# Optimization experiments

Measured on AMD Instinct MI355X. Metric: run time of the kernel, lower is better.

Reference implementation:

```python
import jax, jax.numpy as jnp
import numpy as np

V, T, B = 32000, 64, 32
H, E = 32, 200


def setup_inputs() -> dict:
    key = jax.random.key(0)
    ks = jax.random.split(key, 9)
    s = lambda *d: 1.0 / np.sqrt(d[-1])
    return {
        "y": jax.random.randint(ks[0], (B, T), 0, V, dtype=jnp.int64) if jax.config.jax_enable_x64 else jax.random.randint(ks[0], (B, T), 0, V, dtype=jnp.int32),
        "encoder_last_hidden": jax.random.normal(ks[1], (B, H), dtype=jnp.float32),
        "emb_table": jax.random.normal(ks[2], (V, E), dtype=jnp.float32),
        "Wi": jax.random.uniform(ks[3], (H, E), jnp.float32, -s(E), s(E)),
        "bi": jax.random.uniform(ks[4], (H,), jnp.float32, -s(E), s(E)),
        "Wh": jax.random.uniform(ks[5], (H, H), jnp.float32, -s(H), s(H)),
        "bh": jax.random.uniform(ks[6], (H,), jnp.float32, -s(H), s(H)),
        "Wo": jax.random.uniform(ks[7], (V, H), jnp.float32, -s(H), s(H)),
        "bo": jax.random.uniform(ks[8], (V,), jnp.float32, -s(H), s(H)),
    }


def reference(y, encoder_last_hidden, emb_table, Wi, bi, Wh, bh, Wo, bo):
    # Deterministic teacher forcing (ratio=1.0): input at step t is y[:, t].
    emb = emb_table[y]                      # [B, T, E] embedding gather
    emb_t = jnp.swapaxes(emb, 0, 1)         # [T, B, E] scan over time

    def step(hidden, e):
        # RNNManual cell: tanh(i2h(x) + h2h(h))
        h = jnp.tanh(e @ Wi.T + bi + hidden @ Wh.T + bh)   # [B, H]
        logits = h @ Wo.T + bo                             # [B, V]
        logp = jax.nn.log_softmax(logits, axis=-1)
        pred = jnp.argmax(logp, axis=-1)                   # [B]
        return h, (logp, pred)

    _, (logp, pred) = jax.lax.scan(step, encoder_last_hidden, emb_t)
    logprobs = jnp.swapaxes(logp, 0, 1)     # [B, T, V]
    preds = jnp.swapaxes(pred, 0, 1)        # [B, T] = original `result`
    return logprobs, preds
```

## Files before the change

kernel.cpp:

```cpp
#include <hip/hip_runtime.h>
#include <math.h>

#define BB 32
#define TT 64
#define VV 32000
#define HH 32
#define EE 200
#define MM (BB * TT)
#define MTILES (MM / 16)
#define VC 16
#define VTPC 125
#define NWE (VV * HH)

typedef __attribute__((ext_vector_type(8))) short short8;
typedef __attribute__((ext_vector_type(4))) float f32x4;

__device__ inline void split3(float x, ushort& u0, ushort& u1, ushort& u2) {
    unsigned a = __float_as_uint(x);
    ushort t0 = (ushort)((a + 0x7FFFu + ((a >> 16) & 1u)) >> 16);
    float f0 = __uint_as_float(((unsigned)t0) << 16);
    float r1 = x - f0;
    unsigned b = __float_as_uint(r1);
    ushort t1 = (ushort)((b + 0x7FFFu + ((b >> 16) & 1u)) >> 16);
    float f1 = __uint_as_float(((unsigned)t1) << 16);
    float r2 = r1 - f1;
    unsigned c = __float_as_uint(r2);
    ushort t2 = (ushort)((c + 0x7FFFu + ((c >> 16) & 1u)) >> 16);
    u0 = t0; u1 = t1; u2 = t2;
}

__device__ inline f32x4 mfma6(short8 a0, short8 a1, short8 a2,
                              short8 b0, short8 b1, short8 b2) {
    f32x4 acc = {0.f, 0.f, 0.f, 0.f};
    acc = __builtin_amdgcn_mfma_f32_16x16x32_bf16(a2, b0, acc, 0, 0, 0);
    acc = __builtin_amdgcn_mfma_f32_16x16x32_bf16(a0, b2, acc, 0, 0, 0);
    acc = __builtin_amdgcn_mfma_f32_16x16x32_bf16(a1, b1, acc, 0, 0, 0);
    acc = __builtin_amdgcn_mfma_f32_16x16x32_bf16(a1, b0, acc, 0, 0, 0);
    acc = __builtin_amdgcn_mfma_f32_16x16x32_bf16(a0, b1, acc, 0, 0, 0);
    acc = __builtin_amdgcn_mfma_f32_16x16x32_bf16(a0, b0, acc, 0, 0, 0);
    return acc;
}

__global__ void k_i2h(const int* __restrict__ y, const float* __restrict__ emb,
                      const float* __restrict__ Wi, const float* __restrict__ bi,
                      const float* __restrict__ bh, float* __restrict__ i2h) {
    int bt = blockIdx.x;
    int tok = y[bt];
    __shared__ float se[EE];
    for (int e = threadIdx.x; e < EE; e += blockDim.x) se[e] = emb[(size_t)tok * EE + e];
    __syncthreads();
    int h = threadIdx.x >> 3;
    int j = threadIdx.x & 7;
    float acc = 0.f;
    for (int e = j; e < EE; e += 8) acc += se[e] * Wi[h * EE + e];
    acc += __shfl_down(acc, 4, 8);
    acc += __shfl_down(acc, 2, 8);
    acc += __shfl_down(acc, 1, 8);
    if (j == 0) i2h[bt * HH + h] = acc + bi[h] + bh[h];
}

__global__ void k_rnn(const float* __restrict__ enc, const float* __restrict__ Wh,
                      const float* __restrict__ i2h, float* __restrict__ hall) {
    int b = blockIdx.x;
    int tid = threadIdx.x;
    __shared__ float hs[HH];
    __shared__ float sWh[HH][HH + 1];
    __shared__ float si[TT * HH];
    for (int i = tid; i < HH * HH; i += 64) sWh[i >> 5][i & 31] = Wh[i];
    for (int i = tid; i < TT * HH; i += 64) si[i] = i2h[b * TT * HH + i];
    if (tid < HH) hs[tid] = enc[b * HH + tid];
    __syncthreads();
    for (int t = 0; t < TT; ++t) {
        float hv = 0.f;
        if (tid < HH) {
            float a0 = si[t * HH + tid], a1 = 0.f, a2 = 0.f, a3 = 0.f;
#pragma unroll
            for (int j = 0; j < HH; j += 4) {
                a0 += sWh[tid][j]     * hs[j];
                a1 += sWh[tid][j + 1] * hs[j + 1];
                a2 += sWh[tid][j + 2] * hs[j + 2];
                a3 += sWh[tid][j + 3] * hs[j + 3];
            }
            hv = tanhf((a0 + a1) + (a2 + a3));
        }
        __syncthreads();
        if (tid < HH) {
            hs[tid] = hv;
            hall[(b * TT + t) * HH + tid] = hv;
        }
        __syncthreads();
    }
}

__global__ void k_limbs(const float* __restrict__ Wo, const float* __restrict__ hall,
                        ushort* __restrict__ W0, ushort* __restrict__ W1, ushort* __restrict__ W2,
                        ushort* __restrict__ H0, ushort* __restrict__ H1, ushort* __restrict__ H2) {
    int i = blockIdx.x * 256 + threadIdx.x;
    if (i < NWE) {
        ushort u0, u1, u2; split3(Wo[i], u0, u1, u2);
        W0[i] = u0; W1[i] = u1; W2[i] = u2;
    } else {
        int j = i - NWE;
        if (j >= MM * HH) return;
        ushort u0, u1, u2; split3(hall[j], u0, u1, u2);
        H0[j] = u0; H1[j] = u1; H2[j] = u2;
    }
}

__global__ __launch_bounds__(256) void k_stats_mfma(
        const ushort* __restrict__ W0, const ushort* __restrict__ W1, const ushort* __restrict__ W2,
        const ushort* __restrict__ H0, const ushort* __restrict__ H1, const ushort* __restrict__ H2,
        const float* __restrict__ bo,
        float* __restrict__ pmax, float* __restrict__ pamx, float* __restrict__ psum) {
    int c  = blockIdx.x;
    int wv = threadIdx.x >> 6;
    int l  = threadIdx.x & 63;
    int lc = l & 15, lg = l >> 4;
    int m0 = (blockIdx.y * 4 + wv) * 16;
    size_t aoff = (size_t)(m0 + lc) * HH + lg * 8;
    short8 a0 = *(const short8*)(H0 + aoff);
    short8 a1 = *(const short8*)(H1 + aoff);
    short8 a2 = *(const short8*)(H2 + aoff);

    float mx[4], am[4], sm[4];
#pragma unroll
    for (int q = 0; q < 4; ++q) { mx[q] = -1e30f; am[q] = 0.f; sm[q] = 0.f; }

    int vb = c * (VTPC * 16);
#pragma unroll 5
    for (int s = 0; s < VTPC; ++s) {
        int v = vb + s * 16 + lc;
        size_t boff = (size_t)v * HH + lg * 8;
        short8 b0 = *(const short8*)(W0 + boff);
        short8 b1 = *(const short8*)(W1 + boff);
        short8 b2 = *(const short8*)(W2 + boff);
        f32x4 acc = mfma6(a0, a1, a2, b0, b1, b2);
        float bov = bo[v];
        float vf  = (float)v;
#pragma unroll
        for (int q = 0; q < 4; ++q) {
            float g = acc[q] + bov;
            sm[q] += __expf(g);
            if (g > mx[q]) { mx[q] = g; am[q] = vf; }
        }
    }

#pragma unroll
    for (int q = 0; q < 4; ++q) {
#pragma unroll
        for (int msk = 1; msk <= 8; msk <<= 1) {
            float m2 = __shfl_xor(mx[q], msk);
            float av = __shfl_xor(am[q], msk);
            float s2 = __shfl_xor(sm[q], msk);
            sm[q] += s2;
            if (m2 > mx[q] || (m2 == mx[q] && av < am[q])) { mx[q] = m2; am[q] = av; }
        }
    }
    if (lc == 0) {
        int base = c * MM + m0 + lg * 4;
#pragma unroll
        for (int q = 0; q < 4; ++q) {
            pmax[base + q] = mx[q];
            pamx[base + q] = am[q];
            psum[base + q] = sm[q];
        }
    }
}

__global__ void k_combine(const float* __restrict__ pmax, const float* __restrict__ pamx,
                          const float* __restrict__ psum,
                          float* __restrict__ lse, float* __restrict__ preds) {
    int r = blockIdx.x * blockDim.x + threadIdx.x;
    if (r >= MM) return;
    float m = -1e30f, a = 0.f, s = 0.f;
    for (int c = 0; c < VC; ++c) {
        int idx = c * MM + r;
        float m2 = pmax[idx], a2 = pamx[idx];
        s += psum[idx];
        if (m2 > m || (m2 == m && a2 < a)) { m = m2; a = a2; }
    }
    lse[r] = logf(s);
    preds[r] = a;
}

__global__ __launch_bounds__(64) void k_write_conv(
        const float* __restrict__ Wo,
        const ushort* __restrict__ H0, const ushort* __restrict__ H1, const ushort* __restrict__ H2,
        const float* __restrict__ bo, const float* __restrict__ lse,
        float* __restrict__ out) {
    int v0 = blockIdx.x * 32;
    int lc = threadIdx.x & 15, lg = threadIdx.x >> 4;

    short8 b0a, b1a, b2a, b0b, b1b, b2b;
    {
        const float* ra = Wo + (size_t)(v0 + lc) * HH + lg * 8;
        const float* rb = ra + 16 * HH;
#pragma unroll
        for (int j = 0; j < 8; ++j) {
            ushort u0, u1, u2; split3(ra[j], u0, u1, u2);
            b0a[j] = (short)u0; b1a[j] = (short)u1; b2a[j] = (short)u2;
        }
#pragma unroll
        for (int j = 0; j < 8; ++j) {
            ushort u0, u1, u2; split3(rb[j], u0, u1, u2);
            b0b[j] = (short)u0; b1b[j] = (short)u1; b2b[j] = (short)u2;
        }
    }
    float boA = bo[v0 + lc], boB = bo[v0 + 16 + lc];

    int mbase = blockIdx.y * (MM / 2);
    for (int s = 0; s < MM / 2 / 16; ++s) {
        int m0 = mbase + s * 16;
        size_t aoff = (size_t)(m0 + lc) * HH + lg * 8;
        short8 a0 = *(const short8*)(H0 + aoff);
        short8 a1 = *(const short8*)(H1 + aoff);
        short8 a2 = *(const short8*)(H2 + aoff);
        f32x4 accA = mfma6(a0, a1, a2, b0a, b1a, b2a);
        f32x4 accB = mfma6(a0, a1, a2, b0b, b1b, b2b);
        int row = m0 + lg * 4;
#pragma unroll
        for (int q = 0; q < 4; ++q) {
            float ls = lse[row + q];
            size_t ob = (size_t)(row + q) * VV + v0 + lc;
            out[ob]      = accA[q] + boA - ls;
            out[ob + 16] = accB[q] + boB - ls;
        }
    }
}

extern "C" void kernel_launch(void* const* d_in, const int* in_sizes, int n_in,
                              void* d_out, int out_size, void* d_ws, size_t ws_size,
                              hipStream_t stream) {
    const int*   y   = (const int*)  d_in[0];
    const float* enc = (const float*)d_in[1];
    const float* emb = (const float*)d_in[2];
    const float* Wi  = (const float*)d_in[3];
    const float* bi  = (const float*)d_in[4];
    const float* Wh  = (const float*)d_in[5];
    const float* bh  = (const float*)d_in[6];
    const float* Wo  = (const float*)d_in[7];
    const float* bo  = (const float*)d_in[8];
    float* out = (float*)d_out;
    float* ws  = (float*)d_ws;

    float* i2h  = ws;
    float* hall = ws + 65536;
    float* pmax = ws + 131072;
    float* pamx = ws + 163840;
    float* psum = ws + 196608;
    float* lse  = ws + 229376;
    ushort* Hu  = (ushort*)(ws + 231424);
    ushort* H0 = Hu, *H1 = H0 + MM * HH, *H2 = H1 + MM * HH;

    ushort* Wu = (ushort*)out;
    ushort* W0 = Wu, *W1 = W0 + NWE, *W2 = W1 + NWE;

    k_i2h<<<MM, 256, 0, stream>>>(y, emb, Wi, bi, bh, i2h);
    k_rnn<<<BB, 64, 0, stream>>>(enc, Wh, i2h, hall);
    int tot = NWE + MM * HH;
    k_limbs<<<(tot + 255) / 256, 256, 0, stream>>>(Wo, hall, W0, W1, W2, H0, H1, H2);
    dim3 gs(VC, 32);
    k_stats_mfma<<<gs, 256, 0, stream>>>(W0, W1, W2, H0, H1, H2, bo, pmax, pamx, psum);
    k_combine<<<(MM + 255) / 256, 256, 0, stream>>>(pmax, pamx, psum, lse,
                                                    out + (size_t)MM * VV);
    dim3 gw(1000, 2);
    k_write_conv<<<gw, 64, 0, stream>>>(Wo, H0, H1, H2, bo, lse, out);
}
```

Measured before the change: 465.3 us.

## Fuse Wo limb split into i2h kernel, split hidden limbs in RNN, retile output

Moves the Wo bf16 three-limb split into the i2h pre-kernel as extra blocks, and has the RNN kernel write the hidden-state limbs directly. This removes the separate k_limbs launch and the fp32 hall round trip. The stats kernel vocab chunks change from 16x125 to 25x80 tiles for more blocks. The write kernel doubles its M split and stages lse rows in shared memory. The trade-off is a more complex combined pre-kernel and more partial stats to combine.

After: 430.7 us, median of 2. -7.4%, faster.

```diff
diff --git a/kernel.cpp b/kernel.cpp
--- a/kernel.cpp
+++ b/kernel.cpp
@@ -7,10 +7,10 @@
 #define HH 32
 #define EE 200
 #define MM (BB * TT)
-#define MTILES (MM / 16)
-#define VC 16
-#define VTPC 125
+#define VC 25
+#define VTPC 80
 #define NWE (VV * HH)
+#define WLB ((NWE + 255) / 256)
 
 typedef __attribute__((ext_vector_type(8))) short short8;
 typedef __attribute__((ext_vector_type(4))) float f32x4;
@@ -41,13 +41,24 @@
     return acc;
 }
 
-__global__ void k_i2h(const int* __restrict__ y, const float* __restrict__ emb,
-                      const float* __restrict__ Wi, const float* __restrict__ bi,
-                      const float* __restrict__ bh, float* __restrict__ i2h) {
-    int bt = blockIdx.x;
-    int tok = y[bt];
+__global__ __launch_bounds__(256) void k_pre(
+        const int* __restrict__ y, const float* __restrict__ emb,
+        const float* __restrict__ Wi, const float* __restrict__ bi,
+        const float* __restrict__ bh, const float* __restrict__ Wo,
+        float* __restrict__ i2h,
+        ushort* __restrict__ W0, ushort* __restrict__ W1, ushort* __restrict__ W2) {
+    int blk = blockIdx.x;
+    if (blk >= MM) {
+        int i = (blk - MM) * 256 + (int)threadIdx.x;
+        if (i < NWE) {
+            ushort u0, u1, u2; split3(Wo[i], u0, u1, u2);
+            W0[i] = u0; W1[i] = u1; W2[i] = u2;
+        }
+        return;
+    }
+    int tok = y[blk];
     __shared__ float se[EE];
-    for (int e = threadIdx.x; e < EE; e += blockDim.x) se[e] = emb[(size_t)tok * EE + e];
+    for (int e = threadIdx.x; e < EE; e += 256) se[e] = emb[(size_t)tok * EE + e];
     __syncthreads();
     int h = threadIdx.x >> 3;
     int j = threadIdx.x & 7;
@@ -56,11 +67,13 @@
     acc += __shfl_down(acc, 4, 8);
     acc += __shfl_down(acc, 2, 8);
     acc += __shfl_down(acc, 1, 8);
-    if (j == 0) i2h[bt * HH + h] = acc + bi[h] + bh[h];
+    if (j == 0) i2h[blk * HH + h] = acc + bi[h] + bh[h];
 }
 
 __global__ void k_rnn(const float* __restrict__ enc, const float* __restrict__ Wh,
-                      const float* __restrict__ i2h, float* __restrict__ hall) {
+                      const float* __restrict__ i2h,
+                      ushort* __restrict__ H0, ushort* __restrict__ H1,
+                      ushort* __restrict__ H2) {
     int b = blockIdx.x;
     int tid = threadIdx.x;
     __shared__ float hs[HH];
@@ -86,24 +99,11 @@
         __syncthreads();
         if (tid < HH) {
             hs[tid] = hv;
-            hall[(b * TT + t) * HH + tid] = hv;
+            ushort u0, u1, u2; split3(hv, u0, u1, u2);
+            int idx = (b * TT + t) * HH + tid;
+            H0[idx] = u0; H1[idx] = u1; H2[idx] = u2;
         }
         __syncthreads();
-    }
-}
-
-__global__ void k_limbs(const float* __restrict__ Wo, const float* __restrict__ hall,
-                        ushort* __restrict__ W0, ushort* __restrict__ W1, ushort* __restrict__ W2,
-                        ushort* __restrict__ H0, ushort* __restrict__ H1, ushort* __restrict__ H2) {
-    int i = blockIdx.x * 256 + threadIdx.x;
-    if (i < NWE) {
-        ushort u0, u1, u2; split3(Wo[i], u0, u1, u2);
-        W0[i] = u0; W1[i] = u1; W2[i] = u2;
-    } else {
-        int j = i - NWE;
-        if (j >= MM * HH) return;
-        ushort u0, u1, u2; split3(hall[j], u0, u1, u2);
-        H0[j] = u0; H1[j] = u1; H2[j] = u2;
     }
 }
 
@@ -190,6 +190,10 @@
         float* __restrict__ out) {
     int v0 = blockIdx.x * 32;
     int lc = threadIdx.x & 15, lg = threadIdx.x >> 4;
+    int mbase = blockIdx.y * (MM / 4);
+
+    __shared__ float sl[MM / 4];
+    for (int i = threadIdx.x; i < MM / 4; i += 64) sl[i] = lse[mbase + i];
 
     short8 b0a, b1a, b2a, b0b, b1b, b2b;
     {
@@ -207,9 +211,9 @@
         }
     }
     float boA = bo[v0 + lc], boB = bo[v0 + 16 + lc];
-
-    int mbase = blockIdx.y * (MM / 2);
-    for (int s = 0; s < MM / 2 / 16; ++s) {
+    __syncthreads();
+
+    for (int s = 0; s < MM / 4 / 16; ++s) {
         int m0 = mbase + s * 16;
         size_t aoff = (size_t)(m0 + lc) * HH + lg * 8;
         short8 a0 = *(const short8*)(H0 + aoff);
@@ -218,9 +222,10 @@
         f32x4 accA = mfma6(a0, a1, a2, b0a, b1a, b2a);
         f32x4 accB = mfma6(a0, a1, a2, b0b, b1b, b2b);
         int row = m0 + lg * 4;
+        int lrow = s * 16 + lg * 4;
 #pragma unroll
         for (int q = 0; q < 4; ++q) {
-            float ls = lse[row + q];
+            float ls = sl[lrow + q];
             size_t ob = (size_t)(row + q) * VV + v0 + lc;
             out[ob]      = accA[q] + boA - ls;
             out[ob + 16] = accB[q] + boB - ls;
@@ -244,25 +249,24 @@
     float* ws  = (float*)d_ws;
 
     float* i2h  = ws;
-    float* hall = ws + 65536;
-    float* pmax = ws + 131072;
-    float* pamx = ws + 163840;
-    float* psum = ws + 196608;
-    float* lse  = ws + 229376;
-    ushort* Hu  = (ushort*)(ws + 231424);
-    ushort* H0 = Hu, *H1 = H0 + MM * HH, *H2 = H1 + MM * HH;
-
-    ushort* Wu = (ushort*)out;
-    ushort* W0 = Wu, *W1 = W0 + NWE, *W2 = W1 + NWE;
-
-    k_i2h<<<MM, 256, 0, stream>>>(y, emb, Wi, bi, bh, i2h);
-    k_rnn<<<BB, 64, 0, stream>>>(enc, Wh, i2h, hall);
-    int tot = NWE + MM * HH;
-    k_limbs<<<(tot + 255) / 256, 256, 0, stream>>>(Wo, hall, W0, W1, W2, H0, H1, H2);
+    ushort* H0  = (ushort*)(ws + 65536);
+    ushort* H1  = H0 + MM * HH;
+    ushort* H2  = H1 + MM * HH;
+    float* pmax = ws + 163840;
+    float* pamx = ws + 215040;
+    float* psum = ws + 266240;
+    float* lse  = ws + 317440;
+
+    ushort* W0 = (ushort*)out;
+    ushort* W1 = W0 + NWE;
+    ushort* W2 = W1 + NWE;
+
+    k_pre<<<MM + WLB, 256, 0, stream>>>(y, emb, Wi, bi, bh, Wo, i2h, W0, W1, W2);
+    k_rnn<<<BB, 64, 0, stream>>>(enc, Wh, i2h, H0, H1, H2);
     dim3 gs(VC, 32);
     k_stats_mfma<<<gs, 256, 0, stream>>>(W0, W1, W2, H0, H1, H2, bo, pmax, pamx, psum);
     k_combine<<<(MM + 255) / 256, 256, 0, stream>>>(pmax, pamx, psum, lse,
                                                     out + (size_t)MM * VV);
-    dim3 gw(1000, 2);
+    dim3 gw(1000, 4);
     k_write_conv<<<gw, 64, 0, stream>>>(Wo, H0, H1, H2, bo, lse, out);
 }
```
